# Kernel optimization log

Measured on AMD Instinct MI355X. Metric: run time of the kernel, lower is better.

Reference implementation:

```python
import jax, jax.numpy as jnp
import numpy as np

B, N, C, H = 4, 2048, 1024, 16
HD = C // H  # head dim = 64


def setup_inputs() -> dict:
    key = jax.random.key(0)
    k1, k2, k3, k4 = jax.random.split(key, 4)
    x = jax.random.normal(k1, (B, N, C), dtype=jnp.float32)
    # nn.Linear(C, 3C, bias=False): weight [3C, C], y = x @ W.T
    w_qkv = jax.random.normal(k2, (3 * C, C), dtype=jnp.float32) * (C ** -0.5)
    # nn.Linear(C, C) with bias
    w_out = jax.random.normal(k3, (C, C), dtype=jnp.float32) * (C ** -0.5)
    b_out = jax.random.normal(k4, (C,), dtype=jnp.float32) * 0.01
    return {"x": x, "w_qkv": w_qkv, "w_out": w_out, "b_out": b_out}


def reference(x, w_qkv, w_out, b_out):
    scale = HD ** -0.5
    qkv = jnp.einsum('bnc,dc->bnd', x, w_qkv)  # [B, N, 3C]
    q, k, v = jnp.split(qkv, 3, axis=-1)
    # rearrange 'b n (h c) -> b h n c'
    def heads(t):
        return t.reshape(B, N, H, HD).transpose(0, 2, 1, 3)
    q, k, v = heads(q) * scale, heads(k), heads(v)
    scores = jnp.einsum('bhnc,bhmc->bhnm', q, k)  # [B, H, N, N]
    attn = jax.nn.softmax(scores, axis=-1)
    v_hat = jnp.einsum('bhnm,bhmc->bhnc', attn, v)
    out = v_hat.transpose(0, 2, 1, 3).reshape(B, N, C)  # 'b h n c -> b n (h c)'
    return jnp.einsum('bnc,dc->bnd', out, w_out) + b_out
```

## Files before the change

kernel.cpp:

```cpp
#include <hip/hip_runtime.h>

typedef unsigned short ushort_t;
typedef __attribute__((ext_vector_type(8))) short short8;
typedef __attribute__((ext_vector_type(4))) float f32x4;
typedef __attribute__((ext_vector_type(16))) float f32x16;
typedef __attribute__((ext_vector_type(4))) float float4v;
typedef __attribute__((ext_vector_type(4))) unsigned short ushortx4;
typedef __attribute__((ext_vector_type(4))) unsigned int uint4v;

#define AS1 __attribute__((address_space(1)))
#define AS3 __attribute__((address_space(3)))

#define B_ 4
#define N_ 2048
#define C_ 1024
#define H_ 16
#define HD_ 64
#define M_TOT 8192
#define N3_ 3072

#define QSCALE 0.18033688011112042f

__device__ __forceinline__ unsigned short f2bf(float f) {
    unsigned int u = __float_as_uint(f);
    u += 0x7fffu + ((u >> 16) & 1u);
    return (unsigned short)(u >> 16);
}

__global__ __launch_bounds__(256) void cast_f32_bf16(const float* __restrict__ in,
                                                     ushort_t* __restrict__ out, int n4) {
    int i = blockIdx.x * blockDim.x + threadIdx.x;
    int stride = gridDim.x * blockDim.x;
    for (; i < n4; i += stride) {
        float4v v = ((const float4v*)in)[i];
        ushortx4 o;
        o[0] = f2bf(v[0]); o[1] = f2bf(v[1]); o[2] = f2bf(v[2]); o[3] = f2bf(v[3]);
        ((ushortx4*)out)[i] = o;
    }
}

template <int EPI>
__global__ __launch_bounds__(512, 2) void gemm8p(const ushort_t* __restrict__ A,
                                                 const ushort_t* __restrict__ Bw,
                                                 ushort_t* __restrict__ o0,
                                                 ushort_t* __restrict__ o1,
                                                 ushort_t* __restrict__ o2,
                                                 float* __restrict__ outf,
                                                 const float* __restrict__ bias,
                                                 int K, int NBX) {
    extern __shared__ ushort_t smem[];
    const int tid = threadIdx.x;
    const int lane = tid & 63;
    const int wid = tid >> 6;
    const int l15 = lane & 15, lg = lane >> 4;
    const int wr = wid >> 1;
    const int wc = wid & 1;

    const int wg = blockIdx.x;
    const int id = (wg & 7) * ((int)gridDim.x >> 3) + (wg >> 3);
    const int by = id / NBX, bx = id - by * NBX;
    const int m0 = by * 256, n0 = bx * 128;

    const int koff = (((lane >> 4) ^ ((lane >> 1) & 3)) << 3);
    const int trow = tid >> 2;
    const int slotsrc = (tid & 3) ^ ((tid >> 3) & 3);

    auto stageA = [&](int q, int tt, int kh, int c) {
        const ushort_t* src = A + (size_t)(m0 + c * 128 + trow) * K + tt * 64 + kh * 32 +
                              slotsrc * 8;
        ushort_t* dst = smem + q * 24576 + kh * 8192 + c * 4096 + tid * 8;
        __builtin_amdgcn_global_load_lds((const AS1 void*)src, (AS3 void*)dst, 16, 0, 0);
    };
    auto stageB = [&](int q, int tt, int kh) {
        const ushort_t* src = Bw + (size_t)(n0 + trow) * K + tt * 64 + kh * 32 + slotsrc * 8;
        ushort_t* dst = smem + q * 24576 + 16384 + kh * 4096 + tid * 8;
        __builtin_amdgcn_global_load_lds((const AS1 void*)src, (AS3 void*)dst, 16, 0, 0);
    };

    f32x4 acc[4][4] = {};

    auto phase = [&](int p, int kh) {
        const ushort_t* Ab = smem + p * 24576 + kh * 8192;
        const ushort_t* Bb = smem + p * 24576 + 16384 + kh * 4096;
        short8 af[4], bfr[4];
#pragma unroll
        for (int rt = 0; rt < 4; ++rt)
            af[rt] = *(const short8*)(Ab + (wr * 64 + rt * 16 + l15) * 32 + koff);
#pragma unroll
        for (int ni = 0; ni < 4; ++ni)
            bfr[ni] = *(const short8*)(Bb + (wc * 64 + ni * 16 + l15) * 32 + koff);
        __builtin_amdgcn_s_setprio(1);
#pragma unroll
        for (int rt = 0; rt < 4; ++rt)
#pragma unroll
            for (int ni = 0; ni < 4; ++ni)
                acc[rt][ni] = __builtin_amdgcn_mfma_f32_16x16x32_bf16(af[rt], bfr[ni],
                                                                      acc[rt][ni], 0, 0, 0);
        __builtin_amdgcn_s_setprio(0);
    };

    stageA(0, 0, 0, 0); stageA(0, 0, 0, 1);
    stageA(0, 0, 1, 0); stageA(0, 0, 1, 1);
    stageB(0, 0, 0);    stageB(0, 0, 1);

    const int NT = K >> 6;
    for (int t = 0; t < NT; ++t) {
        const int p = t & 1, q = p ^ 1;
        if (t + 1 < NT) {
            stageA(q, t + 1, 0, 0); stageA(q, t + 1, 0, 1);
            __builtin_amdgcn_sched_barrier(0);
            asm volatile("s_waitcnt vmcnt(2)");
        } else {
            asm volatile("s_waitcnt vmcnt(0)");
        }
        __builtin_amdgcn_sched_barrier(0);
        __builtin_amdgcn_s_barrier();
        __builtin_amdgcn_sched_barrier(0);
        phase(p, 0);
        if (t + 1 < NT) {
            stageA(q, t + 1, 1, 0); stageA(q, t + 1, 1, 1);
            stageB(q, t + 1, 0);    stageB(q, t + 1, 1);
        }
        __builtin_amdgcn_sched_barrier(0);
        __builtin_amdgcn_s_barrier();
        __builtin_amdgcn_sched_barrier(0);
        phase(p, 1);
    }

    if (EPI == 0) {
        const int sel = bx >> 3;
#pragma unroll
        for (int mi = 0; mi < 4; ++mi) {
            const int r0 = m0 + wr * 64 + mi * 16 + lg * 4;
            const int b = r0 >> 11, n = r0 & 2047;
            const int blk = n >> 5, nlo = n & 31;
#pragma unroll
            for (int ni = 0; ni < 4; ++ni) {
                const int cq = (bx & 7) * 128 + wc * 64 + ni * 16 + l15;
                const int h = cq >> 6, hd = cq & 63;
                const int bh = b * H_ + h;
                f32x4 a = acc[mi][ni];
                if (sel == 2) {
                    size_t base = (((size_t)(bh * 64 + blk) * 2 + (hd >> 5)) * 2 +
                                   ((n >> 4) & 1)) * 512 +
                                  ((hd & 31) + ((n >> 3) & 1) * 32) * 8 + (n & 7);
                    ushortx4 pk;
#pragma unroll
                    for (int j = 0; j < 4; ++j) pk[j] = f2bf(a[j]);
                    *(ushortx4*)(&o2[base]) = pk;
                } else {
                    size_t base = ((size_t)(bh * 64 + blk) * 4 + (hd >> 4)) * 512 +
                                  (nlo + ((hd >> 3) & 1) * 32) * 8 + (hd & 7);
                    if (sel == 0) {
#pragma unroll
                        for (int j = 0; j < 4; ++j) o0[base + j * 8] = f2bf(a[j] * QSCALE);
                    } else {
#pragma unroll
                        for (int j = 0; j < 4; ++j) o1[base + j * 8] = f2bf(a[j]);
                    }
                }
            }
        }
    } else {
#pragma unroll
        for (int ni = 0; ni < 4; ++ni) {
            const int c = n0 + wc * 64 + ni * 16 + l15;
            const float bv = bias[c];
#pragma unroll
            for (int mi = 0; mi < 4; ++mi) {
                const int r0 = m0 + wr * 64 + mi * 16 + lg * 4;
                f32x4 a = acc[mi][ni];
#pragma unroll
                for (int j = 0; j < 4; ++j)
                    outf[(size_t)(r0 + j) * C_ + c] = a[j] + bv;
            }
        }
    }
}

__global__ __launch_bounds__(256, 2) void attn_fwd(const ushort_t* __restrict__ Qf,
                                                   const ushort_t* __restrict__ Kf,
                                                   const ushort_t* __restrict__ Vf,
                                                   ushort_t* __restrict__ Ov) {
    const int tid = threadIdx.x;
    const int lane = tid & 63;
    const int wid = tid >> 6;
    const int lc = lane & 31, lh = lane >> 5;

    const int wg = blockIdx.x;
    const int xcd = wg & 7, slot = wg >> 3;
    const int bh = xcd * 8 + (slot >> 3);
    const int qt = slot & 7;

    const ushort_t* qpb = Qf + (size_t)bh * N_ * HD_;
    const ushort_t* kpb = Kf + (size_t)bh * N_ * HD_;
    const ushort_t* vpb = Vf + (size_t)bh * N_ * HD_;

    const int qblk0 = qt * 8 + wid * 2;

    short8 qf[2][4];
#pragma unroll
    for (int qc = 0; qc < 2; ++qc)
#pragma unroll
        for (int ks = 0; ks < 4; ++ks)
            qf[qc][ks] = *(const short8*)(qpb + ((size_t)(qblk0 + qc) * 4 + ks) * 512 +
                                          lane * 8);

    f32x16 oacc[2][2] = {};
    float srun[2] = {0.f, 0.f};

    short8 kfA[4], kfB[4], vfA[4], vfB[4];
#pragma unroll
    for (int ks = 0; ks < 4; ++ks)
        kfA[ks] = *(const short8*)(kpb + (size_t)ks * 512 + lane * 8);
#pragma unroll
    for (int dt = 0; dt < 2; ++dt)
#pragma unroll
        for (int kb = 0; kb < 2; ++kb)
            vfA[dt * 2 + kb] = *(const short8*)(vpb + ((size_t)dt * 2 + kb) * 512 + lane * 8);

    auto iter = [&](short8(&kfu)[4], short8(&kfp)[4], short8(&vfu)[4], short8(&vfp)[4],
                    int t) {
        f32x16 sacc[2] = {};
        __builtin_amdgcn_s_setprio(1);
#pragma unroll
        for (int ks = 0; ks < 4; ++ks)
#pragma unroll
            for (int qc = 0; qc < 2; ++qc)
                sacc[qc] = __builtin_amdgcn_mfma_f32_32x32x16_bf16(kfu[ks], qf[qc][ks],
                                                                   sacc[qc], 0, 0, 0);
        __builtin_amdgcn_s_setprio(0);

        const int kvn = (t + 1) & 63;
#pragma unroll
        for (int ks = 0; ks < 4; ++ks)
            kfp[ks] = *(const short8*)(kpb + ((size_t)kvn * 4 + ks) * 512 + lane * 8);
#pragma unroll
        for (int dt = 0; dt < 2; ++dt)
#pragma unroll
            for (int kb = 0; kb < 2; ++kb)
                vfp[dt * 2 + kb] = *(const short8*)(vpb + (((size_t)kvn * 2 + dt) * 2 + kb) *
                                                    512 + lane * 8);

#pragma unroll
        for (int qc = 0; qc < 2; ++qc) {
            float p[16];
#pragma unroll
            for (int r = 0; r < 16; ++r) p[r] = __builtin_amdgcn_exp2f(sacc[qc][r]);
            float s01 = (p[0] + p[1]) + (p[2] + p[3]);
            float s23 = (p[4] + p[5]) + (p[6] + p[7]);
            float s45 = (p[8] + p[9]) + (p[10] + p[11]);
            float s67 = (p[12] + p[13]) + (p[14] + p[15]);
            srun[qc] += (s01 + s23) + (s45 + s67);

            unsigned pk[4][2];
#pragma unroll
            for (int r1 = 0; r1 < 4; ++r1)
#pragma unroll
                for (int c = 0; c < 2; ++c)
                    asm("v_cvt_pk_bf16_f32 %0, %1, %2"
                        : "=v"(pk[r1][c])
                        : "v"(p[4 * r1 + 2 * c]), "v"(p[4 * r1 + 2 * c + 1]));

            short8 pb[2];
#pragma unroll
            for (int kb = 0; kb < 2; ++kb) {
                unsigned a0 = pk[2 * kb][0], b0 = pk[2 * kb + 1][0];
                unsigned a1 = pk[2 * kb][1], b1 = pk[2 * kb + 1][1];
                asm("v_permlane32_swap_b32 %0, %1" : "+v"(a0), "+v"(b0));
                asm("v_permlane32_swap_b32 %0, %1" : "+v"(a1), "+v"(b1));
                uint4v w;
                w[0] = a0; w[1] = a1; w[2] = b0; w[3] = b1;
                pb[kb] = __builtin_bit_cast(short8, w);
            }

            __builtin_amdgcn_s_setprio(1);
#pragma unroll
            for (int dt = 0; dt < 2; ++dt)
#pragma unroll
                for (int kb = 0; kb < 2; ++kb)
                    oacc[qc][dt] = __builtin_amdgcn_mfma_f32_32x32x16_bf16(
                        vfu[dt * 2 + kb], pb[kb], oacc[qc][dt], 0, 0, 0);
            __builtin_amdgcn_s_setprio(0);
        }
    };

    for (int t2 = 0; t2 < 64; t2 += 2) {
        iter(kfA, kfB, vfA, vfB, t2);
        iter(kfB, kfA, vfB, vfA, t2 + 1);
    }

    const int b = bh >> 4, h = bh & 15;
#pragma unroll
    for (int qc = 0; qc < 2; ++qc) {
        float s = srun[qc];
        s += __shfl_xor(s, 32, 64);
        const float inv = 1.f / s;
        const int qg = (qblk0 + qc) * 32 + lc;
        ushort_t* orow = Ov + (size_t)(b * N_ + qg) * C_ + h * HD_;
#pragma unroll
        for (int dt = 0; dt < 2; ++dt)
#pragma unroll
            for (int r1 = 0; r1 < 4; ++r1) {
                ushortx4 pkv;
#pragma unroll
                for (int r0 = 0; r0 < 4; ++r0)
                    pkv[r0] = f2bf(oacc[qc][dt][4 * r1 + r0] * inv);
                *(ushortx4*)(orow + dt * 32 + r1 * 8 + lh * 4) = pkv;
            }
    }
}

extern "C" void kernel_launch(void* const* d_in, const int* in_sizes, int n_in,
                              void* d_out, int out_size, void* d_ws, size_t ws_size,
                              hipStream_t stream) {
    const float* x = (const float*)d_in[0];
    const float* wqkv = (const float*)d_in[1];
    const float* wout = (const float*)d_in[2];
    const float* bout = (const float*)d_in[3];
    float* out = (float*)d_out;

    ushort_t* ws = (ushort_t*)d_ws;
    const size_t XN = (size_t)M_TOT * C_;
    const size_t WQN = (size_t)N3_ * C_;
    const size_t WON = (size_t)C_ * C_;
    ushort_t* xbf = ws;
    ushort_t* wqkvb = xbf + XN;
    ushort_t* woutb = wqkvb + WQN;
    ushort_t* karr = woutb + WON;
    ushort_t* varr = karr + XN;
    ushort_t* qarr = varr + XN;
    ushort_t* vhat = xbf;

    cast_f32_bf16<<<2048, 256, 0, stream>>>(x, xbf, (int)(XN / 4));
    cast_f32_bf16<<<1024, 256, 0, stream>>>(wqkv, wqkvb, (int)(WQN / 4));
    cast_f32_bf16<<<512, 256, 0, stream>>>(wout, woutb, (int)(WON / 4));

    gemm8p<0><<<768, 512, 98304, stream>>>(xbf, wqkvb, qarr, karr, varr,
                                           nullptr, nullptr, C_, 24);
    attn_fwd<<<512, 256, 0, stream>>>(qarr, karr, varr, vhat);
    gemm8p<1><<<256, 512, 98304, stream>>>(vhat, woutb, nullptr, nullptr, nullptr,
                                           out, bout, C_, 8);
}
```

Before: 180.1 us.

## Shrink GEMM tiles to 4 waves, fuse cast kernels, sum softmax via MFMA

```diff
diff --git a/kernel.cpp b/kernel.cpp
--- a/kernel.cpp
+++ b/kernel.cpp
@@ -27,20 +27,33 @@
     return (unsigned short)(u >> 16);
 }
 
-__global__ __launch_bounds__(256) void cast_f32_bf16(const float* __restrict__ in,
-                                                     ushort_t* __restrict__ out, int n4) {
+__global__ __launch_bounds__(256) void cast3_f32_bf16(const float* __restrict__ xa,
+                                                      const float* __restrict__ xb,
+                                                      const float* __restrict__ xc,
+                                                      ushort_t* __restrict__ oa,
+                                                      ushort_t* __restrict__ ob,
+                                                      ushort_t* __restrict__ oc,
+                                                      int n4a, int n4b, int n4c) {
     int i = blockIdx.x * blockDim.x + threadIdx.x;
-    int stride = gridDim.x * blockDim.x;
-    for (; i < n4; i += stride) {
-        float4v v = ((const float4v*)in)[i];
+    const int stride = gridDim.x * blockDim.x;
+    const int tot = n4a + n4b + n4c;
+    for (; i < tot; i += stride) {
+        const float4v* src;
+        ushortx4* dst;
+        int j = i;
+        if (j < n4a) { src = (const float4v*)xa; dst = (ushortx4*)oa; }
+        else if ((j -= n4a) < n4b) { src = (const float4v*)xb; dst = (ushortx4*)ob; }
+        else { j -= n4b; src = (const float4v*)xc; dst = (ushortx4*)oc; }
+        float4v v = src[j];
         ushortx4 o;
         o[0] = f2bf(v[0]); o[1] = f2bf(v[1]); o[2] = f2bf(v[2]); o[3] = f2bf(v[3]);
-        ((ushortx4*)out)[i] = o;
-    }
-}
+        dst[j] = o;
+    }
+}
+
 
 template <int EPI>
-__global__ __launch_bounds__(512, 2) void gemm8p(const ushort_t* __restrict__ A,
+__global__ __launch_bounds__(256, 2) void gemm4w(const ushort_t* __restrict__ A,
                                                  const ushort_t* __restrict__ Bw,
                                                  ushort_t* __restrict__ o0,
                                                  ushort_t* __restrict__ o1,
@@ -48,40 +61,45 @@
                                                  float* __restrict__ outf,
                                                  const float* __restrict__ bias,
                                                  int K, int NBX) {
-    extern __shared__ ushort_t smem[];
+    __shared__ ushort_t smem[2][16384];
     const int tid = threadIdx.x;
     const int lane = tid & 63;
     const int wid = tid >> 6;
     const int l15 = lane & 15, lg = lane >> 4;
-    const int wr = wid >> 1;
-    const int wc = wid & 1;
+    const int wr = wid >> 1, wc = wid & 1;
 
     const int wg = blockIdx.x;
     const int id = (wg & 7) * ((int)gridDim.x >> 3) + (wg >> 3);
     const int by = id / NBX, bx = id - by * NBX;
-    const int m0 = by * 256, n0 = bx * 128;
-
-    const int koff = (((lane >> 4) ^ ((lane >> 1) & 3)) << 3);
-    const int trow = tid >> 2;
+    const int m0 = by * 128, n0 = bx * 128;
+
+    const int koff = ((lg ^ ((lane >> 1) & 3)) << 3);
     const int slotsrc = (tid & 3) ^ ((tid >> 3) & 3);
 
-    auto stageA = [&](int q, int tt, int kh, int c) {
-        const ushort_t* src = A + (size_t)(m0 + c * 128 + trow) * K + tt * 64 + kh * 32 +
-                              slotsrc * 8;
-        ushort_t* dst = smem + q * 24576 + kh * 8192 + c * 4096 + tid * 8;
-        __builtin_amdgcn_global_load_lds((const AS1 void*)src, (AS3 void*)dst, 16, 0, 0);
+    auto stageA = [&](int q, int tt, int kh) {
+#pragma unroll
+        for (int j = 0; j < 2; ++j) {
+            const ushort_t* src = A + (size_t)(m0 + j * 64 + (tid >> 2)) * K + tt * 64 +
+                                  kh * 32 + slotsrc * 8;
+            ushort_t* dst = &smem[q][kh * 4096 + j * 2048 + tid * 8];
+            __builtin_amdgcn_global_load_lds((const AS1 void*)src, (AS3 void*)dst, 16, 0, 0);
+        }
     };
     auto stageB = [&](int q, int tt, int kh) {
-        const ushort_t* src = Bw + (size_t)(n0 + trow) * K + tt * 64 + kh * 32 + slotsrc * 8;
-        ushort_t* dst = smem + q * 24576 + 16384 + kh * 4096 + tid * 8;
-        __builtin_amdgcn_global_load_lds((const AS1 void*)src, (AS3 void*)dst, 16, 0, 0);
+#pragma unroll
+        for (int j = 0; j < 2; ++j) {
+            const ushort_t* src = Bw + (size_t)(n0 + j * 64 + (tid >> 2)) * K + tt * 64 +
+                                  kh * 32 + slotsrc * 8;
+            ushort_t* dst = &smem[q][8192 + kh * 4096 + j * 2048 + tid * 8];
+            __builtin_amdgcn_global_load_lds((const AS1 void*)src, (AS3 void*)dst, 16, 0, 0);
+        }
     };
 
     f32x4 acc[4][4] = {};
 
     auto phase = [&](int p, int kh) {
-        const ushort_t* Ab = smem + p * 24576 + kh * 8192;
-        const ushort_t* Bb = smem + p * 24576 + 16384 + kh * 4096;
+        const ushort_t* Ab = &smem[p][kh * 4096];
+        const ushort_t* Bb = &smem[p][8192 + kh * 4096];
         short8 af[4], bfr[4];
 #pragma unroll
         for (int rt = 0; rt < 4; ++rt)
@@ -99,17 +117,16 @@
         __builtin_amdgcn_s_setprio(0);
     };
 
-    stageA(0, 0, 0, 0); stageA(0, 0, 0, 1);
-    stageA(0, 0, 1, 0); stageA(0, 0, 1, 1);
-    stageB(0, 0, 0);    stageB(0, 0, 1);
+    stageA(0, 0, 0); stageB(0, 0, 0);
+    stageA(0, 0, 1); stageB(0, 0, 1);
 
     const int NT = K >> 6;
     for (int t = 0; t < NT; ++t) {
         const int p = t & 1, q = p ^ 1;
         if (t + 1 < NT) {
-            stageA(q, t + 1, 0, 0); stageA(q, t + 1, 0, 1);
+            stageA(q, t + 1, 0); stageB(q, t + 1, 0);
             __builtin_amdgcn_sched_barrier(0);
-            asm volatile("s_waitcnt vmcnt(2)");
+            asm volatile("s_waitcnt vmcnt(4)");
         } else {
             asm volatile("s_waitcnt vmcnt(0)");
         }
@@ -118,8 +135,7 @@
         __builtin_amdgcn_sched_barrier(0);
         phase(p, 0);
         if (t + 1 < NT) {
-            stageA(q, t + 1, 1, 0); stageA(q, t + 1, 1, 1);
-            stageB(q, t + 1, 0);    stageB(q, t + 1, 1);
+            stageA(q, t + 1, 1); stageB(q, t + 1, 1);
         }
         __builtin_amdgcn_sched_barrier(0);
         __builtin_amdgcn_s_barrier();
@@ -207,7 +223,11 @@
                                           lane * 8);
 
     f32x16 oacc[2][2] = {};
-    float srun[2] = {0.f, 0.f};
+    f32x16 ssum[2] = {};
+
+    uint4v ow;
+    ow[0] = 0x3F803F80u; ow[1] = 0x3F803F80u; ow[2] = 0x3F803F80u; ow[3] = 0x3F803F80u;
+    const short8 onesf = __builtin_bit_cast(short8, ow);
 
     short8 kfA[4], kfB[4], vfA[4], vfB[4];
 #pragma unroll
@@ -247,11 +267,6 @@
             float p[16];
 #pragma unroll
             for (int r = 0; r < 16; ++r) p[r] = __builtin_amdgcn_exp2f(sacc[qc][r]);
-            float s01 = (p[0] + p[1]) + (p[2] + p[3]);
-            float s23 = (p[4] + p[5]) + (p[6] + p[7]);
-            float s45 = (p[8] + p[9]) + (p[10] + p[11]);
-            float s67 = (p[12] + p[13]) + (p[14] + p[15]);
-            srun[qc] += (s01 + s23) + (s45 + s67);
 
             unsigned pk[4][2];
 #pragma unroll
@@ -275,6 +290,10 @@
             }
 
             __builtin_amdgcn_s_setprio(1);
+            ssum[qc] = __builtin_amdgcn_mfma_f32_32x32x16_bf16(onesf, pb[0], ssum[qc],
+                                                               0, 0, 0);
+            ssum[qc] = __builtin_amdgcn_mfma_f32_32x32x16_bf16(onesf, pb[1], ssum[qc],
+                                                               0, 0, 0);
 #pragma unroll
             for (int dt = 0; dt < 2; ++dt)
 #pragma unroll
@@ -293,9 +312,7 @@
     const int b = bh >> 4, h = bh & 15;
 #pragma unroll
     for (int qc = 0; qc < 2; ++qc) {
-        float s = srun[qc];
-        s += __shfl_xor(s, 32, 64);
-        const float inv = 1.f / s;
+        const float inv = 1.f / ssum[qc][0];
         const int qg = (qblk0 + qc) * 32 + lc;
         ushort_t* orow = Ov + (size_t)(b * N_ + qg) * C_ + h * HD_;
 #pragma unroll
@@ -332,13 +349,12 @@
     ushort_t* qarr = varr + XN;
     ushort_t* vhat = xbf;
 
-    cast_f32_bf16<<<2048, 256, 0, stream>>>(x, xbf, (int)(XN / 4));
-    cast_f32_bf16<<<1024, 256, 0, stream>>>(wqkv, wqkvb, (int)(WQN / 4));
-    cast_f32_bf16<<<512, 256, 0, stream>>>(wout, woutb, (int)(WON / 4));
-
-    gemm8p<0><<<768, 512, 98304, stream>>>(xbf, wqkvb, qarr, karr, varr,
-                                           nullptr, nullptr, C_, 24);
+    cast3_f32_bf16<<<2048, 256, 0, stream>>>(x, wqkv, wout, xbf, wqkvb, woutb,
+                                             (int)(XN / 4), (int)(WQN / 4), (int)(WON / 4));
+
+    gemm4w<0><<<1536, 256, 0, stream>>>(xbf, wqkvb, qarr, karr, varr,
+                                        nullptr, nullptr, C_, 24);
     attn_fwd<<<512, 256, 0, stream>>>(qarr, karr, varr, vhat);
-    gemm8p<1><<<256, 512, 98304, stream>>>(vhat, woutb, nullptr, nullptr, nullptr,
-                                           out, bout, C_, 8);
-}
+    gemm4w<1><<<512, 256, 0, stream>>>(vhat, woutb, nullptr, nullptr, nullptr,
+                                       out, bout, C_, 8);
+}
```

New measurement: 188.5 us. 4.7% more time.
